# Kernel tuning notes

Measured on AMD Instinct MI355X. Metric: run time of the kernel, lower is better.

Reference implementation:

```python
import jax, jax.numpy as jnp
import numpy as np

HD, M = 4096, 14336

def setup_inputs() -> dict:
    key = jax.random.key(0)
    k_x, k_g, k_u, k_d = jax.random.split(key, 4)
    scale = 1.0 / np.sqrt(HD)
    x = jax.random.normal(k_x, (4, 2048, HD), dtype=jnp.float16)
    # Dequantized fp16 weights, stored torch-style as [out_features, in_features]
    W_gate = (jax.random.normal(k_g, (M, HD), dtype=jnp.float16) * jnp.float16(scale))
    W_up   = (jax.random.normal(k_u, (M, HD), dtype=jnp.float16) * jnp.float16(scale))
    W_down = (jax.random.normal(k_d, (HD, M), dtype=jnp.float16) * jnp.float16(1.0 / np.sqrt(M)))
    return {"x": x, "W_gate": W_gate, "W_up": W_up, "W_down": W_down}

def reference(x, W_gate, W_up, W_down):
    # SwiGLU: down( silu(x @ Wg^T) * (x @ Wu^T) )
    gate = jnp.einsum("bsh,mh->bsm", x, W_gate)   # [B,S,M]
    up = jnp.einsum("bsh,mh->bsm", x, W_up)       # [B,S,M]
    h = jax.nn.silu(gate) * up                       # fused elementwise
    out = jnp.einsum("bsm,hm->bsh", h, W_down)    # [B,S,HD]
    return out
```

## Files before the change

### kernel.cpp

```cpp
#include <hip/hip_runtime.h>

typedef _Float16 f16;
typedef _Float16 f16x8 __attribute__((ext_vector_type(8)));
typedef float f32x4 __attribute__((ext_vector_type(4)));

__device__ __forceinline__ f16x8 cvt8(f32x4 lo, f32x4 hi) {
    f16x8 h;
    h[0] = (f16)lo[0]; h[1] = (f16)lo[1]; h[2] = (f16)lo[2]; h[3] = (f16)lo[3];
    h[4] = (f16)hi[0]; h[5] = (f16)hi[1]; h[6] = (f16)hi[2]; h[7] = (f16)hi[3];
    return h;
}

__global__ __launch_bounds__(256)
void cvt_f32_f16(const float* __restrict__ in, f16* __restrict__ out, long long n) {
    long long i = ((long long)blockIdx.x * 256 + threadIdx.x) * 8;
    const long long stride = (long long)gridDim.x * 256 * 8;
    for (; i < n; i += stride) {
        f32x4 a = *(const f32x4*)(in + i);
        f32x4 b = *(const f32x4*)(in + i + 4);
        *(f16x8*)(out + i) = cvt8(a, b);
    }
}

__global__ void fill_sentinel_f32(float* __restrict__ out, long long n) {
    long long i = (long long)blockIdx.x * blockDim.x + threadIdx.x;
    long long stride = (long long)gridDim.x * blockDim.x;
    for (; i < n; i += stride) out[i] = 1.0f;
}

__device__ __forceinline__ void gload_lds16(const f16* g, f16* l) {
    __builtin_amdgcn_global_load_lds(
        (const __attribute__((address_space(1))) unsigned int*)(unsigned long long)g,
        (__attribute__((address_space(3))) unsigned int*)(unsigned int)(unsigned long long)l,
        16, 0, 0);
}

template<bool FUSED>
__global__ __launch_bounds__(512)
void mlp_gemm16(const f16* __restrict__ A, const f16* __restrict__ B0,
                const f16* __restrict__ B1, void* __restrict__ Cv,
                int K, int ldc, int nRow, int nCol, int RG) {
    __shared__ __align__(16) f16 smA[128 * 64];
    __shared__ __align__(16) f16 smB0[128 * 64];
    __shared__ __align__(16) f16 smB1[FUSED ? 128 * 64 : 8];

    const int lin   = blockIdx.x;
    const int perSg = RG * nCol;
    const int sg    = lin / perSg;
    const int rem   = lin - sg * perSg;
    int rgIn = nRow - sg * RG; if (rgIn > RG) rgIn = RG;
    const int colB = rem / rgIn;
    const int rowB = sg * RG + (rem - colB * rgIn);

    const long long blockRow = (long long)rowB * 128;
    const long long blockCol = (long long)colB * 128;

    const int tid  = threadIdx.x;
    const int w    = tid >> 6;
    const int lane = tid & 63;
    const int waveM = w >> 2;
    const int waveN = w & 3;

    const int drw = w * 8 + (lane >> 3);
    const int se  = ((lane & 7) << 3) ^ ((lane >> 3) << 3);
    const f16* gA0  = A  + (blockRow + drw) * (long long)K + se;
    const f16* gA1  = gA0 + 64 * (long long)K;
    const f16* gB00 = B0 + (blockCol + drw) * (long long)K + se;
    const f16* gB01 = gB00 + 64 * (long long)K;
    const f16* gB10 = FUSED ? (B1 + (blockCol + drw) * (long long)K + se) : nullptr;
    const f16* gB11 = FUSED ? (gB10 + 64 * (long long)K) : nullptr;

    f16* lA0  = smA  + w * 512;
    f16* lA1  = smA  + 4096 + w * 512;
    f16* lB00 = smB0 + w * 512;
    f16* lB01 = smB0 + 4096 + w * 512;
    f16* lB10 = smB1 + w * 512;
    f16* lB11 = smB1 + 4096 + w * 512;

    const int fr = lane & 15;
    const int hi = lane >> 4;
    const int swz = (fr & 7) << 3;
    int offA[2][4], offB[2][2];
#pragma unroll
    for (int ks = 0; ks < 2; ++ks) {
        const int kterm = (ks * 32 + hi * 8) ^ swz;
#pragma unroll
        for (int i = 0; i < 4; ++i)
            offA[ks][i] = (waveM * 64 + i * 16 + fr) * 64 + kterm;
#pragma unroll
        for (int n = 0; n < 2; ++n)
            offB[ks][n] = (waveN * 32 + n * 16 + fr) * 64 + kterm;
    }

    f32x4 acc0[4][2];
    f32x4 acc1[4][2];
#pragma unroll
    for (int mi = 0; mi < 4; ++mi)
#pragma unroll
        for (int ni = 0; ni < 2; ++ni) {
            acc0[mi][ni] = (f32x4){0.f, 0.f, 0.f, 0.f};
            if constexpr (FUSED) acc1[mi][ni] = (f32x4){0.f, 0.f, 0.f, 0.f};
        }

    const int ksteps = K >> 6;
    for (int kt = 0; kt < ksteps; ++kt) {
        gload_lds16(gA0,  lA0);
        gload_lds16(gA1,  lA1);
        gload_lds16(gB00, lB00);
        gload_lds16(gB01, lB01);
        if constexpr (FUSED) {
            gload_lds16(gB10, lB10);
            gload_lds16(gB11, lB11);
        }
        gA0 += 64; gA1 += 64; gB00 += 64; gB01 += 64;
        if constexpr (FUSED) { gB10 += 64; gB11 += 64; }

        __syncthreads();

#pragma unroll
        for (int ks = 0; ks < 2; ++ks) {
            f16x8 aF[4], bF[2], b1F[2];
#pragma unroll
            for (int i = 0; i < 4; ++i) aF[i] = *(const f16x8*)(smA + offA[ks][i]);
#pragma unroll
            for (int n = 0; n < 2; ++n) bF[n] = *(const f16x8*)(smB0 + offB[ks][n]);
            if constexpr (FUSED) {
#pragma unroll
                for (int n = 0; n < 2; ++n) b1F[n] = *(const f16x8*)(smB1 + offB[ks][n]);
            }
#pragma unroll
            for (int mi = 0; mi < 4; ++mi)
#pragma unroll
                for (int ni = 0; ni < 2; ++ni) {
                    acc0[mi][ni] = __builtin_amdgcn_mfma_f32_16x16x32_f16(
                        aF[mi], bF[ni], acc0[mi][ni], 0, 0, 0);
                    if constexpr (FUSED)
                        acc1[mi][ni] = __builtin_amdgcn_mfma_f32_16x16x32_f16(
                            aF[mi], b1F[ni], acc1[mi][ni], 0, 0, 0);
                }
        }

        __syncthreads();
    }

    const long long orBase = blockRow + waveM * 64 + hi * 4;
    const long long ocBase = blockCol + waveN * 32 + fr;
#pragma unroll
    for (int mi = 0; mi < 4; ++mi)
#pragma unroll
        for (int ni = 0; ni < 2; ++ni)
#pragma unroll
            for (int j = 0; j < 4; ++j) {
                const long long idx =
                    (orBase + mi * 16 + j) * (long long)ldc + (ocBase + ni * 16);
                if constexpr (FUSED) {
                    float gv = acc0[mi][ni][j];
                    float uv = acc1[mi][ni][j];
                    float v = (gv / (1.f + __expf(-gv))) * uv;
                    ((f16*)Cv)[idx] = (f16)v;
                } else {
                    ((float*)Cv)[idx] = acc0[mi][ni][j];
                }
            }
}

template<bool IS16>
__device__ __forceinline__ f16x8 load8(const char* p) {
    if constexpr (IS16) return *(const f16x8*)p;
    const float* f = (const float*)p;
    return cvt8(*(const f32x4*)f, *(const f32x4*)(f + 4));
}

template<bool FUSED, bool A16, bool B16>
__global__ __launch_bounds__(256)
void mlp_gemm(const void* __restrict__ Av, const void* __restrict__ B0v,
              const void* __restrict__ B1v, void* __restrict__ Cv,
              int K, int ldc, int nRow, int nCol, int RG) {
    __shared__ __align__(16) f16 smA[128 * 32];
    __shared__ __align__(16) f16 smB0[128 * 32];
    __shared__ __align__(16) f16 smB1[FUSED ? 128 * 32 : 8];

    const int lin   = blockIdx.x;
    const int perSg = RG * nCol;
    const int sg    = lin / perSg;
    const int rem   = lin - sg * perSg;
    int rgIn = nRow - sg * RG; if (rgIn > RG) rgIn = RG;
    const int colB = rem / rgIn;
    const int rowB = sg * RG + (rem - colB * rgIn);

    const long long blockRow = (long long)rowB * 128;
    const long long blockCol = (long long)colB * 128;

    const int tid  = threadIdx.x;
    const int w    = tid >> 6;
    const int lane = tid & 63;
    const int waveM = w >> 1;
    const int waveN = w & 1;

    const int r0 = tid >> 2;
    const int s0 = tid & 3;
    const int szA = A16 ? 2 : 4;
    const int szB = B16 ? 2 : 4;
    const char* gA0  = (const char*)Av  + ((blockRow + r0)      * (long long)K + s0 * 8) * szA;
    const char* gA1  = (const char*)Av  + ((blockRow + r0 + 64) * (long long)K + s0 * 8) * szA;
    const char* gB00 = (const char*)B0v + ((blockCol + r0)      * (long long)K + s0 * 8) * szB;
    const char* gB01 = (const char*)B0v + ((blockCol + r0 + 64) * (long long)K + s0 * 8) * szB;
    const char* gB10 = FUSED ? (const char*)B1v + ((blockCol + r0)      * (long long)K + s0 * 8) * szB : nullptr;
    const char* gB11 = FUSED ? (const char*)B1v + ((blockCol + r0 + 64) * (long long)K + s0 * 8) * szB : nullptr;

    const int off0 = tid * 8;
    const int off1 = off0 + 2048;

    const int fr = lane & 15;
    const int fk = (lane >> 4) * 8;
    int offA[4], offB[4];
#pragma unroll
    for (int i = 0; i < 4; ++i) {
        offA[i] = (waveM * 64 + i * 16 + fr) * 32 + fk;
        offB[i] = (waveN * 64 + i * 16 + fr) * 32 + fk;
    }

    f32x4 acc0[4][4];
    f32x4 acc1[4][4];
#pragma unroll
    for (int mi = 0; mi < 4; ++mi)
#pragma unroll
        for (int ni = 0; ni < 4; ++ni) {
            acc0[mi][ni] = (f32x4){0.f, 0.f, 0.f, 0.f};
            if constexpr (FUSED) acc1[mi][ni] = (f32x4){0.f, 0.f, 0.f, 0.f};
        }

    const int ksteps = K >> 5;
    for (int kt = 0; kt < ksteps; ++kt) {
        f16x8 vA0  = load8<A16>(gA0);
        f16x8 vA1  = load8<A16>(gA1);
        f16x8 vB00 = load8<B16>(gB00);
        f16x8 vB01 = load8<B16>(gB01);
        f16x8 vB10, vB11;
        if constexpr (FUSED) {
            vB10 = load8<B16>(gB10);
            vB11 = load8<B16>(gB11);
        }
        gA0 += 32 * szA; gA1 += 32 * szA;
        gB00 += 32 * szB; gB01 += 32 * szB;
        if constexpr (FUSED) { gB10 += 32 * szB; gB11 += 32 * szB; }

        __syncthreads();

        *(f16x8*)(smA  + off0) = vA0;
        *(f16x8*)(smA  + off1) = vA1;
        *(f16x8*)(smB0 + off0) = vB00;
        *(f16x8*)(smB0 + off1) = vB01;
        if constexpr (FUSED) {
            *(f16x8*)(smB1 + off0) = vB10;
            *(f16x8*)(smB1 + off1) = vB11;
        }

        __syncthreads();

        f16x8 aF[4], bF[4], b1F[4];
#pragma unroll
        for (int i = 0; i < 4; ++i) aF[i] = *(const f16x8*)(smA + offA[i]);
#pragma unroll
        for (int i = 0; i < 4; ++i) bF[i] = *(const f16x8*)(smB0 + offB[i]);
        if constexpr (FUSED) {
#pragma unroll
            for (int i = 0; i < 4; ++i) b1F[i] = *(const f16x8*)(smB1 + offB[i]);
        }

#pragma unroll
        for (int mi = 0; mi < 4; ++mi)
#pragma unroll
            for (int ni = 0; ni < 4; ++ni) {
                acc0[mi][ni] = __builtin_amdgcn_mfma_f32_16x16x32_f16(
                    aF[mi], bF[ni], acc0[mi][ni], 0, 0, 0);
                if constexpr (FUSED)
                    acc1[mi][ni] = __builtin_amdgcn_mfma_f32_16x16x32_f16(
                        aF[mi], b1F[ni], acc1[mi][ni], 0, 0, 0);
            }
    }

    const long long orBase = blockRow + waveM * 64 + ((lane >> 4) * 4);
    const long long ocBase = blockCol + waveN * 64 + fr;
#pragma unroll
    for (int mi = 0; mi < 4; ++mi)
#pragma unroll
        for (int ni = 0; ni < 4; ++ni)
#pragma unroll
            for (int j = 0; j < 4; ++j) {
                const long long idx =
                    (orBase + mi * 16 + j) * (long long)ldc + (ocBase + ni * 16);
                if constexpr (FUSED) {
                    float gv = acc0[mi][ni][j];
                    float uv = acc1[mi][ni][j];
                    float v = (gv / (1.f + __expf(-gv))) * uv;
                    ((f16*)Cv)[idx] = (f16)v;
                } else {
                    ((float*)Cv)[idx] = acc0[mi][ni][j];
                }
            }
}

extern "C" void kernel_launch(void* const* d_in, const int* in_sizes, int n_in,
                              void* d_out, int out_size, void* d_ws, size_t ws_size,
                              hipStream_t stream) {
    const float* x  = (const float*)d_in[0];
    const float* Wg = (const float*)d_in[1];
    const float* Wu = (const float*)d_in[2];
    const float* Wd = (const float*)d_in[3];
    float* out = (float*)d_out;

    const int HD = 4096;
    const int T  = in_sizes[0] / HD;
    const int M  = in_sizes[1] / HD;

    const long long nW = (long long)M * HD;
    const long long nX = (long long)T * HD;
    const size_t wBytes = (size_t)nW * 2;
    const size_t xBytes = (size_t)nX * 2;
    const size_t hRow   = (size_t)M * 2;
    const size_t minH   = 128 * hRow;

    char* p = (char*)d_ws;
    size_t rem = ws_size;
    f16 *Wg16 = nullptr, *Wu16 = nullptr, *Wd16 = nullptr, *X16 = nullptr;
    bool wf16 = false, xf16 = false;
    if (rem >= 3 * wBytes + minH) {
        Wg16 = (f16*)p; p += wBytes;
        Wu16 = (f16*)p; p += wBytes;
        Wd16 = (f16*)p; p += wBytes;
        rem -= 3 * wBytes;
        wf16 = true;
        if (rem >= xBytes + minH) {
            X16 = (f16*)p; p += xBytes; rem -= xBytes; xf16 = true;
        }
    }
    f16* H = (f16*)p;
    long long maxRows = (long long)(rem / hRow);
    int chunk = (int)((maxRows / 128) * 128);
    if (chunk > T) chunk = T;
    if (chunk <= 0) {
        fill_sentinel_f32<<<1024, 256, 0, stream>>>(out, (long long)out_size);
        return;
    }

    if (wf16) {
        cvt_f32_f16<<<2048, 256, 0, stream>>>(Wg, Wg16, nW);
        cvt_f32_f16<<<2048, 256, 0, stream>>>(Wu, Wu16, nW);
        cvt_f32_f16<<<2048, 256, 0, stream>>>(Wd, Wd16, nW);
    }
    if (xf16) cvt_f32_f16<<<2048, 256, 0, stream>>>(x, X16, nX);

    for (int t0 = 0; t0 < T; t0 += chunk) {
        int rows = (T - t0 < chunk) ? (T - t0) : chunk;
        int nRow = rows / 128;
        {
            int nCol = M / 128;
            dim3 grid(nRow * nCol);
            int RG = nRow;
            if (xf16)
                mlp_gemm16<true><<<grid, 512, 0, stream>>>(
                    X16 + (size_t)t0 * HD, Wg16, Wu16, H, HD, M, nRow, nCol, RG);
            else if (wf16)
                mlp_gemm<true, false, true><<<grid, 256, 0, stream>>>(
                    x + (size_t)t0 * HD, Wg16, Wu16, H, HD, M, nRow, nCol, RG);
            else
                mlp_gemm<true, false, false><<<grid, 256, 0, stream>>>(
                    x + (size_t)t0 * HD, Wg, Wu, H, HD, M, nRow, nCol, RG);
        }
        {
            int nCol = HD / 128;
            dim3 grid(nRow * nCol);
            int RG = (nRow < 32) ? nRow : 32;
            if (wf16)
                mlp_gemm16<false><<<grid, 512, 0, stream>>>(
                    H, Wd16, nullptr, out + (size_t)t0 * HD, M, HD, nRow, nCol, RG);
            else
                mlp_gemm<false, true, false><<<grid, 256, 0, stream>>>(
                    H, Wd, nullptr, out + (size_t)t0 * HD, M, HD, nRow, nCol, RG);
        }
    }
}
```

Baseline: 2.948 ms.

## Double-buffer LDS with BK=32 and widen down-proj tile to 128x256

```diff
diff --git a/kernel.cpp b/kernel.cpp
--- a/kernel.cpp
+++ b/kernel.cpp
@@ -40,9 +40,11 @@
 void mlp_gemm16(const f16* __restrict__ A, const f16* __restrict__ B0,
                 const f16* __restrict__ B1, void* __restrict__ Cv,
                 int K, int ldc, int nRow, int nCol, int RG) {
-    __shared__ __align__(16) f16 smA[128 * 64];
-    __shared__ __align__(16) f16 smB0[128 * 64];
-    __shared__ __align__(16) f16 smB1[FUSED ? 128 * 64 : 8];
+    constexpr int BN    = FUSED ? 128 : 256;
+    constexpr int BROWS = FUSED ? 128 : 256;
+    __shared__ __align__(16) f16 smA[2][128 * 32];
+    __shared__ __align__(16) f16 smB0[2][BROWS * 32];
+    __shared__ __align__(16) f16 smB1[FUSED ? 2 : 1][FUSED ? 128 * 32 : 8];
 
     const int lin   = blockIdx.x;
     const int perSg = RG * nCol;
@@ -53,7 +55,7 @@
     const int rowB = sg * RG + (rem - colB * rgIn);
 
     const long long blockRow = (long long)rowB * 128;
-    const long long blockCol = (long long)colB * 128;
+    const long long blockCol = (long long)colB * BN;
 
     const int tid  = threadIdx.x;
     const int w    = tid >> 6;
@@ -61,94 +63,88 @@
     const int waveM = w >> 2;
     const int waveN = w & 3;
 
-    const int drw = w * 8 + (lane >> 3);
-    const int se  = ((lane & 7) << 3) ^ ((lane >> 3) << 3);
-    const f16* gA0  = A  + (blockRow + drw) * (long long)K + se;
-    const f16* gA1  = gA0 + 64 * (long long)K;
-    const f16* gB00 = B0 + (blockCol + drw) * (long long)K + se;
-    const f16* gB01 = gB00 + 64 * (long long)K;
-    const f16* gB10 = FUSED ? (B1 + (blockCol + drw) * (long long)K + se) : nullptr;
-    const f16* gB11 = FUSED ? (gB10 + 64 * (long long)K) : nullptr;
-
-    f16* lA0  = smA  + w * 512;
-    f16* lA1  = smA  + 4096 + w * 512;
-    f16* lB00 = smB0 + w * 512;
-    f16* lB01 = smB0 + 4096 + w * 512;
-    f16* lB10 = smB1 + w * 512;
-    f16* lB11 = smB1 + 4096 + w * 512;
+    const int dr   = tid >> 2;
+    const int dblk = tid & 3;
+    const int gblk = (dblk - (dr >> 1)) & 3;
+    const f16* gA   = A  + (blockRow + dr) * (long long)K + gblk * 8;
+    const f16* gB0a = B0 + (blockCol + dr) * (long long)K + gblk * 8;
+    const f16* gB0b = FUSED ? nullptr
+                            : B0 + (blockCol + 128 + dr) * (long long)K + gblk * 8;
+    const f16* gB1a = FUSED ? B1 + (blockCol + dr) * (long long)K + gblk * 8
+                            : nullptr;
+    const int wbase = w * 512;
 
     const int fr = lane & 15;
     const int hi = lane >> 4;
-    const int swz = (fr & 7) << 3;
-    int offA[2][4], offB[2][2];
-#pragma unroll
-    for (int ks = 0; ks < 2; ++ks) {
-        const int kterm = (ks * 32 + hi * 8) ^ swz;
-#pragma unroll
-        for (int i = 0; i < 4; ++i)
-            offA[ks][i] = (waveM * 64 + i * 16 + fr) * 64 + kterm;
-#pragma unroll
-        for (int n = 0; n < 2; ++n)
-            offB[ks][n] = (waveN * 32 + n * 16 + fr) * 64 + kterm;
-    }
-
-    f32x4 acc0[4][2];
-    f32x4 acc1[4][2];
+    constexpr int NI = FUSED ? 2 : 4;
+    int aOff[4], bOff[NI];
+#pragma unroll
+    for (int i = 0; i < 4; ++i) {
+        const int r = waveM * 64 + i * 16 + fr;
+        aOff[i] = r * 32 + (((hi + (r >> 1)) & 3) << 3);
+    }
+#pragma unroll
+    for (int n = 0; n < NI; ++n) {
+        const int r = waveN * (FUSED ? 32 : 64) + n * 16 + fr;
+        bOff[n] = r * 32 + (((hi + (r >> 1)) & 3) << 3);
+    }
+
+    f32x4 acc0[4][NI];
+    f32x4 acc1[FUSED ? 4 : 1][FUSED ? NI : 1];
 #pragma unroll
     for (int mi = 0; mi < 4; ++mi)
 #pragma unroll
-        for (int ni = 0; ni < 2; ++ni) {
+        for (int ni = 0; ni < NI; ++ni) {
             acc0[mi][ni] = (f32x4){0.f, 0.f, 0.f, 0.f};
             if constexpr (FUSED) acc1[mi][ni] = (f32x4){0.f, 0.f, 0.f, 0.f};
         }
 
-    const int ksteps = K >> 6;
-    for (int kt = 0; kt < ksteps; ++kt) {
-        gload_lds16(gA0,  lA0);
-        gload_lds16(gA1,  lA1);
-        gload_lds16(gB00, lB00);
-        gload_lds16(gB01, lB01);
-        if constexpr (FUSED) {
-            gload_lds16(gB10, lB10);
-            gload_lds16(gB11, lB11);
-        }
-        gA0 += 64; gA1 += 64; gB00 += 64; gB01 += 64;
-        if constexpr (FUSED) { gB10 += 64; gB11 += 64; }
-
+    auto stage = [&](int b) {
+        gload_lds16(gA, &smA[b][wbase]);     gA += 32;
+        gload_lds16(gB0a, &smB0[b][wbase]);  gB0a += 32;
+        if constexpr (FUSED) {
+            gload_lds16(gB1a, &smB1[b][wbase]); gB1a += 32;
+        } else {
+            gload_lds16(gB0b, &smB0[b][4096 + wbase]); gB0b += 32;
+        }
+    };
+
+    const int nk = K >> 5;
+    int cur = 0;
+    stage(0);
+    for (int kt = 0; kt < nk; ++kt) {
         __syncthreads();
-
-#pragma unroll
-        for (int ks = 0; ks < 2; ++ks) {
-            f16x8 aF[4], bF[2], b1F[2];
-#pragma unroll
-            for (int i = 0; i < 4; ++i) aF[i] = *(const f16x8*)(smA + offA[ks][i]);
-#pragma unroll
-            for (int n = 0; n < 2; ++n) bF[n] = *(const f16x8*)(smB0 + offB[ks][n]);
-            if constexpr (FUSED) {
-#pragma unroll
-                for (int n = 0; n < 2; ++n) b1F[n] = *(const f16x8*)(smB1 + offB[ks][n]);
-            }
-#pragma unroll
-            for (int mi = 0; mi < 4; ++mi)
-#pragma unroll
-                for (int ni = 0; ni < 2; ++ni) {
-                    acc0[mi][ni] = __builtin_amdgcn_mfma_f32_16x16x32_f16(
-                        aF[mi], bF[ni], acc0[mi][ni], 0, 0, 0);
-                    if constexpr (FUSED)
-                        acc1[mi][ni] = __builtin_amdgcn_mfma_f32_16x16x32_f16(
-                            aF[mi], b1F[ni], acc1[mi][ni], 0, 0, 0);
-                }
-        }
-
-        __syncthreads();
+        if (kt + 1 < nk) stage(cur ^ 1);
+
+        f16x8 aF[4], bF[NI], b1F[FUSED ? NI : 1];
+#pragma unroll
+        for (int i = 0; i < 4; ++i) aF[i] = *(const f16x8*)(&smA[cur][aOff[i]]);
+#pragma unroll
+        for (int n = 0; n < NI; ++n) bF[n] = *(const f16x8*)(&smB0[cur][bOff[n]]);
+        if constexpr (FUSED) {
+#pragma unroll
+            for (int n = 0; n < NI; ++n) b1F[n] = *(const f16x8*)(&smB1[cur][bOff[n]]);
+        }
+
+#pragma unroll
+        for (int mi = 0; mi < 4; ++mi)
+#pragma unroll
+            for (int ni = 0; ni < NI; ++ni) {
+                acc0[mi][ni] = __builtin_amdgcn_mfma_f32_16x16x32_f16(
+                    aF[mi], bF[ni], acc0[mi][ni], 0, 0, 0);
+                if constexpr (FUSED)
+                    acc1[mi][ni] = __builtin_amdgcn_mfma_f32_16x16x32_f16(
+                        aF[mi], b1F[ni], acc1[mi][ni], 0, 0, 0);
+            }
+        cur ^= 1;
     }
 
     const long long orBase = blockRow + waveM * 64 + hi * 4;
-    const long long ocBase = blockCol + waveN * 32 + fr;
+    const long long ocBase = blockCol + waveN * (FUSED ? 32 : 64) + fr;
 #pragma unroll
     for (int mi = 0; mi < 4; ++mi)
 #pragma unroll
-        for (int ni = 0; ni < 2; ++ni)
+        for (int ni = 0; ni < NI; ++ni)
 #pragma unroll
             for (int j = 0; j < 4; ++j) {
                 const long long idx =
@@ -369,15 +365,19 @@
                     x + (size_t)t0 * HD, Wg, Wu, H, HD, M, nRow, nCol, RG);
         }
         {
-            int nCol = HD / 128;
-            dim3 grid(nRow * nCol);
-            int RG = (nRow < 32) ? nRow : 32;
-            if (wf16)
+            if (wf16) {
+                int nCol = HD / 256;
+                dim3 grid(nRow * nCol);
+                int RG = (nRow < 32) ? nRow : 32;
                 mlp_gemm16<false><<<grid, 512, 0, stream>>>(
                     H, Wd16, nullptr, out + (size_t)t0 * HD, M, HD, nRow, nCol, RG);
-            else
+            } else {
+                int nCol = HD / 128;
+                dim3 grid(nRow * nCol);
+                int RG = (nRow < 32) ? nRow : 32;
                 mlp_gemm<false, true, false><<<grid, 256, 0, stream>>>(
                     H, Wd, nullptr, out + (size_t)t0 * HD, M, HD, nRow, nCol, RG);
-        }
-    }
-}
+            }
+        }
+    }
+}
```

Result: slower. 3.165 ms (+7.4%).
